# Performance work log

Hardware: AMD Instinct MI355X
Metric: run time of the kernel (lower is better)

Reference implementation:

```python
import jax, jax.numpy as jnp
import numpy as np

B, N, K = 4, 8192, 16
D_POINTS, D_MODEL, INIT_DIM = 64, 64, 3

def _lin(key, din, dout, bias=True):
    k1, k2 = jax.random.split(key)
    s = 1.0 / np.sqrt(din)
    w = jax.random.uniform(k1, (din, dout), minval=-s, maxval=s, dtype=jnp.float32)
    if not bias:
        return w
    b = jax.random.uniform(k2, (dout,), minval=-s, maxval=s, dtype=jnp.float32)
    return w, b

def setup_inputs() -> dict:
    key = jax.random.key(0)
    ks = jax.random.split(key, 12)
    xyz = jax.random.normal(ks[0], (B, N, INIT_DIM), dtype=jnp.float32)
    features = jax.random.normal(ks[1], (B, N, D_POINTS), dtype=jnp.float32)
    knn_idx = jax.random.randint(ks[2], (B, N, K), 0, N)
    fc1_w, fc1_b = _lin(ks[3], D_POINTS, D_MODEL)
    fc2_w, fc2_b = _lin(ks[4], D_MODEL, D_POINTS)
    d1_w, d1_b = _lin(ks[5], INIT_DIM, D_MODEL)
    d2_w, d2_b = _lin(ks[6], D_MODEL, D_MODEL)
    g1_w, g1_b = _lin(ks[7], D_MODEL, D_MODEL)
    g2_w, g2_b = _lin(ks[8], D_MODEL, D_MODEL)
    wq = _lin(ks[9], D_MODEL, D_MODEL, bias=False)
    wk = _lin(ks[10], D_MODEL, D_MODEL, bias=False)
    wv = _lin(ks[11], D_MODEL, D_MODEL, bias=False)
    return dict(xyz=xyz, features=features, knn_idx=knn_idx,
                fc1_w=fc1_w, fc1_b=fc1_b, fc2_w=fc2_w, fc2_b=fc2_b,
                d1_w=d1_w, d1_b=d1_b, d2_w=d2_w, d2_b=d2_b,
                g1_w=g1_w, g1_b=g1_b, g2_w=g2_w, g2_b=g2_b,
                wq=wq, wk=wk, wv=wv)

def _index_points(x, idx):
    # x: (B, N, D), idx: (B, M, K) -> (B, M, K, D)
    return jax.vmap(lambda xb, ib: xb[ib])(x, idx)

def reference(xyz, features, knn_idx,
              fc1_w, fc1_b, fc2_w, fc2_b,
              d1_w, d1_b, d2_w, d2_b,
              g1_w, g1_b, g2_w, g2_b,
              wq, wk, wv):
    idx = knn_idx[:, :, :K]
    knn_xyz = _index_points(xyz, idx)                      # (B,N,K,3)
    pre = features
    x = features @ fc1_w + fc1_b                           # (B,N,d_model)
    q = x @ wq                                             # (B,N,d_model)
    k = _index_points(x @ wk, idx)                         # (B,N,K,d_model)
    v = _index_points(x @ wv, idx)                         # (B,N,K,d_model)
    rel = xyz[:, :, None, :] - knn_xyz                     # (B,N,K,3)
    pos_enc = jax.nn.relu(rel @ d1_w + d1_b) @ d2_w + d2_b # (B,N,K,d_model)
    h = q[:, :, None, :] - k + pos_enc
    attn = jax.nn.relu(h @ g1_w + g1_b) @ g2_w + g2_b      # (B,N,K,d_model)
    attn = jax.nn.softmax(attn / np.sqrt(D_MODEL), axis=-2)
    res = jnp.einsum('bmnf,bmnf->bmf', attn, v + pos_enc)  # (B,N,d_model)
    res = res @ fc2_w + fc2_b + pre                        # (B,N,d_points)
    return res, attn
```

## Files before the change

kernel.cpp:

```cpp
#include <hip/hip_runtime.h>
#include <hip/hip_bf16.h>

#define B_    4
#define N_    8192
#define TOT   (B_*N_)
#define KNN_  16
#define PPW   8
#define PITCH 80

typedef _Float16 half8  __attribute__((ext_vector_type(8)));
typedef float    floatx4 __attribute__((ext_vector_type(4)));

#define MFMA16(A, Bv, C) __builtin_amdgcn_mfma_f32_16x16x32_f16((A), (Bv), (C), 0, 0, 0)

__device__ __forceinline__ void lds_fence(){
  asm volatile("s_waitcnt lgkmcnt(0)" ::: "memory");
}
__device__ __forceinline__ half8 h8_load_f32(const float* __restrict__ p){
  float4 a = *(const float4*)p;
  float4 b = *(const float4*)(p + 4);
  half8 r;
  r[0] = (_Float16)a.x; r[1] = (_Float16)a.y; r[2] = (_Float16)a.z; r[3] = (_Float16)a.w;
  r[4] = (_Float16)b.x; r[5] = (_Float16)b.y; r[6] = (_Float16)b.z; r[7] = (_Float16)b.w;
  return r;
}
__device__ __forceinline__ void store8f(float* __restrict__ p, half8 v){
  float4 a = {(float)v[0], (float)v[1], (float)v[2], (float)v[3]};
  float4 b = {(float)v[4], (float)v[5], (float)v[6], (float)v[7]};
  *(float4*)p = a;
  *(float4*)(p + 4) = b;
}

__device__ void fill_w64(half8* dst, const float* __restrict__ W, int tid){
  for (int i = tid; i < 512; i += 256){
    int lane = i & 63, nt = (i >> 6) & 3, kt = i >> 8;
    int n  = nt*16 + (lane & 15);
    int kb = kt*32 + ((lane >> 4) & 3)*8;
    half8 v;
    #pragma unroll
    for (int j = 0; j < 8; j++) v[j] = (_Float16)W[(kb + j)*64 + n];
    dst[i] = v;
  }
}

__global__ __launch_bounds__(256, 3) void k1_qkv(
    const float* __restrict__ feat, const float* __restrict__ fc1w, const float* __restrict__ fc1b,
    const float* __restrict__ wqw, const float* __restrict__ wkw, const float* __restrict__ wvw,
    _Float16* __restrict__ qws, _Float16* __restrict__ kws, _Float16* __restrict__ vws)
{
  __shared__ half8 Sfc1[512], Sq[512], Sk[512], Sv[512];
  __shared__ alignas(16) _Float16 xt[4][16*PITCH];
  const int tid = threadIdx.x;
  fill_w64(Sfc1, fc1w, tid);
  fill_w64(Sq, wqw, tid);
  fill_w64(Sk, wkw, tid);
  fill_w64(Sv, wvw, tid);
  __syncthreads();

  const int wave = tid >> 6, lane = tid & 63, quad = lane >> 4, m16 = lane & 15;
  _Float16* tx = &xt[wave][0];
  const int rowbase = blockIdx.x*64 + wave*16;
  float fb[4];
  #pragma unroll
  for (int nt = 0; nt < 4; nt++) fb[nt] = fc1b[nt*16 + m16];

  const int arow = rowbase + m16;
  half8 Fa0 = h8_load_f32(&feat[arow*64 + quad*8]);
  half8 Fa1 = h8_load_f32(&feat[arow*64 + 32 + quad*8]);
  const floatx4 z4 = {0.f, 0.f, 0.f, 0.f};

  #pragma unroll
  for (int nt = 0; nt < 4; nt++){
    floatx4 acc = MFMA16(Fa0, Sfc1[nt*64 + lane], z4);
    acc = MFMA16(Fa1, Sfc1[(4 + nt)*64 + lane], acc);
    const int col = nt*16 + m16;
    #pragma unroll
    for (int r = 0; r < 4; r++)
      tx[(quad*4 + r)*PITCH + col] = (_Float16)(acc[r] + fb[nt]);
  }
  lds_fence();
  const half8 Ax0 = *(const half8*)&tx[m16*PITCH + quad*8];
  const half8 Ax1 = *(const half8*)&tx[m16*PITCH + 32 + quad*8];

#define EMIT_QKV(S, OUT)                                                      \
  { _Pragma("unroll")                                                         \
    for (int nt = 0; nt < 4; nt++){                                           \
      floatx4 acc = MFMA16(Ax0, S[nt*64 + lane], z4);                         \
      acc = MFMA16(Ax1, S[(4 + nt)*64 + lane], acc);                          \
      _Pragma("unroll")                                                       \
      for (int r = 0; r < 4; r++)                                             \
        OUT[(rowbase + quad*4 + r)*64 + nt*16 + m16] = (_Float16)acc[r];      \
    } }
  EMIT_QKV(Sq, qws)
  EMIT_QKV(Sk, kws)
  EMIT_QKV(Sv, vws)
#undef EMIT_QKV
}

__global__ __launch_bounds__(256, 2) void k2_point(
    const float* __restrict__ xyz, const int* __restrict__ knn,
    const float* __restrict__ d1w, const float* __restrict__ d1b,
    const float* __restrict__ d2w, const float* __restrict__ d2b,
    const float* __restrict__ g1w, const float* __restrict__ g1b,
    const float* __restrict__ g2w, const float* __restrict__ g2b,
    const _Float16* __restrict__ qws, const _Float16* __restrict__ kws,
    const _Float16* __restrict__ vws,
    _Float16* __restrict__ r0, float* __restrict__ attn_out)
{
  __shared__ half8 Sd2[512], Sg1[512], Sg2[512];
  __shared__ float4 Td1[64];
  __shared__ alignas(16) _Float16 tiles[4][2][16*PITCH];
  const int tid = threadIdx.x;
  fill_w64(Sd2, d2w, tid);
  fill_w64(Sg1, g1w, tid);
  fill_w64(Sg2, g2w, tid);
  if (tid < 64)
    Td1[tid] = make_float4(d1w[tid], d1w[64 + tid], d1w[128 + tid], d1b[tid]);
  __syncthreads();

  const int wave = tid >> 6, lane = tid & 63, quad = lane >> 4, m16 = lane & 15;
  _Float16* tT0 = &tiles[wave][0][0];
  _Float16* tT1 = &tiles[wave][1][0];

  half8 Fd2[2][4], Fg1[2][4], Fg2[2][4];
  #pragma unroll
  for (int nt = 0; nt < 4; nt++){
    #pragma unroll
    for (int kt = 0; kt < 2; kt++){
      Fd2[kt][nt] = Sd2[(kt*4 + nt)*64 + lane];
      Fg1[kt][nt] = Sg1[(kt*4 + nt)*64 + lane];
      Fg2[kt][nt] = Sg2[(kt*4 + nt)*64 + lane];
    }
  }
  float bd2[4], bg1[4], bg2[4];
  #pragma unroll
  for (int nt = 0; nt < 4; nt++){
    const int c = nt*16 + m16;
    bd2[nt] = d2b[c]; bg1[nt] = g1b[c]; bg2[nt] = g2b[c];
  }
  const floatx4 z4 = {0.f, 0.f, 0.f, 0.f};
  const int wsw = quad << 3;
  const int swz = (quad ^ (m16 >> 2)) << 3;

  const int swb  = (blockIdx.x & 7)*128 + (blockIdx.x >> 3);
  const int gpt0 = swb*(4*PPW) + wave*PPW;
  const int b    = gpt0 >> 13;

  int growA = b*N_ + knn[gpt0*KNN_ + m16];
  int growB = b*N_ + knn[(gpt0+1)*KNN_ + m16];
  float xqA0 = xyz[gpt0*3+0],     xqA1 = xyz[gpt0*3+1],     xqA2 = xyz[gpt0*3+2];
  float xqB0 = xyz[(gpt0+1)*3+0], xqB1 = xyz[(gpt0+1)*3+1], xqB2 = xyz[(gpt0+1)*3+2];
  float xnA0 = xyz[growA*3+0], xnA1 = xyz[growA*3+1], xnA2 = xyz[growA*3+2];
  float xnB0 = xyz[growB*3+0], xnB1 = xyz[growB*3+1], xnB2 = xyz[growB*3+2];

  for (int pp = 0; pp < PPW; pp += 2){
    const int gptA = gpt0 + pp, gptB = gptA + 1;
    const int gA = growA, gB = growB;

    const half8 KaA0 = *(const half8*)&kws[gA*64 + quad*8];
    const half8 KaA1 = *(const half8*)&kws[gA*64 + 32 + quad*8];
    const half8 QaA0 = *(const half8*)&qws[gptA*64 + quad*8];
    const half8 QaA1 = *(const half8*)&qws[gptA*64 + 32 + quad*8];
    const half8 VaA0 = *(const half8*)&vws[gA*64 + quad*8];
    const half8 VaA1 = *(const half8*)&vws[gA*64 + 32 + quad*8];
    const half8 KaB0 = *(const half8*)&kws[gB*64 + quad*8];
    const half8 KaB1 = *(const half8*)&kws[gB*64 + 32 + quad*8];
    const half8 QaB0 = *(const half8*)&qws[gptB*64 + quad*8];
    const half8 QaB1 = *(const half8*)&qws[gptB*64 + 32 + quad*8];
    const half8 VaB0 = *(const half8*)&vws[gB*64 + quad*8];
    const half8 VaB1 = *(const half8*)&vws[gB*64 + 32 + quad*8];

    int growA_n = 0, growB_n = 0;
    if (pp < PPW-2){
      growA_n = b*N_ + knn[(gptA+2)*KNN_ + m16];
      growB_n = b*N_ + knn[(gptB+2)*KNN_ + m16];
    }

    const float dxA = xqA0 - xnA0, dyA = xqA1 - xnA1, dzA = xqA2 - xnA2;
    const float dxB = xqB0 - xnB0, dyB = xqB1 - xnB1, dzB = xqB2 - xnB2;

    half8 AtA0, AtA1, AtB0, AtB1;
    #pragma unroll
    for (int j = 0; j < 8; j++){
      const float4 w  = Td1[quad*8 + j];
      const float4 w2 = Td1[32 + quad*8 + j];
      float tA  = fmaf(dxA, w.x,  fmaf(dyA, w.y,  fmaf(dzA, w.z,  w.w)));
      float tA2 = fmaf(dxA, w2.x, fmaf(dyA, w2.y, fmaf(dzA, w2.z, w2.w)));
      float tB  = fmaf(dxB, w.x,  fmaf(dyB, w.y,  fmaf(dzB, w.z,  w.w)));
      float tB2 = fmaf(dxB, w2.x, fmaf(dyB, w2.y, fmaf(dzB, w2.z, w2.w)));
      AtA0[j] = (_Float16)(tA  > 0.f ? tA  : 0.f);
      AtA1[j] = (_Float16)(tA2 > 0.f ? tA2 : 0.f);
      AtB0[j] = (_Float16)(tB  > 0.f ? tB  : 0.f);
      AtB1[j] = (_Float16)(tB2 > 0.f ? tB2 : 0.f);
    }

    #pragma unroll
    for (int nt = 0; nt < 4; nt++){
      floatx4 accA = MFMA16(AtA0, Fd2[0][nt], z4);
      accA = MFMA16(AtA1, Fd2[1][nt], accA);
      floatx4 accB = MFMA16(AtB0, Fd2[0][nt], z4);
      accB = MFMA16(AtB1, Fd2[1][nt], accB);
      const int colS = (nt*16 + m16) ^ wsw;
      #pragma unroll
      for (int r = 0; r < 4; r++){
        tT0[(quad*4 + r)*PITCH + colS] = (_Float16)(accA[r] + bd2[nt]);
        tT1[(quad*4 + r)*PITCH + colS] = (_Float16)(accB[r] + bd2[nt]);
      }
    }
    lds_fence();
    const half8 PaA0 = *(const half8*)&tT0[m16*PITCH + swz];
    const half8 PaA1 = *(const half8*)&tT0[m16*PITCH + 32 + swz];
    const half8 PaB0 = *(const half8*)&tT1[m16*PITCH + swz];
    const half8 PaB1 = *(const half8*)&tT1[m16*PITCH + 32 + swz];
    const half8 HA0 = QaA0 - KaA0 + PaA0;
    const half8 HA1 = QaA1 - KaA1 + PaA1;
    const half8 HB0 = QaB0 - KaB0 + PaB0;
    const half8 HB1 = QaB1 - KaB1 + PaB1;

    #pragma unroll
    for (int nt = 0; nt < 4; nt++){
      floatx4 accA = MFMA16(HA0, Fg1[0][nt], z4);
      accA = MFMA16(HA1, Fg1[1][nt], accA);
      floatx4 accB = MFMA16(HB0, Fg1[0][nt], z4);
      accB = MFMA16(HB1, Fg1[1][nt], accB);
      const int colS = (nt*16 + m16) ^ wsw;
      #pragma unroll
      for (int r = 0; r < 4; r++){
        float tA = accA[r] + bg1[nt];
        float tB = accB[r] + bg1[nt];
        tT0[(quad*4 + r)*PITCH + colS] = (_Float16)(tA > 0.f ? tA : 0.f);
        tT1[(quad*4 + r)*PITCH + colS] = (_Float16)(tB > 0.f ? tB : 0.f);
      }
    }
    lds_fence();
    const half8 UA0 = *(const half8*)&tT0[m16*PITCH + swz];
    const half8 UA1 = *(const half8*)&tT0[m16*PITCH + 32 + swz];
    const half8 UB0 = *(const half8*)&tT1[m16*PITCH + swz];
    const half8 UB1 = *(const half8*)&tT1[m16*PITCH + 32 + swz];

    float A2A[4][4], A2B[4][4];
    #pragma unroll
    for (int nt = 0; nt < 4; nt++){
      floatx4 accA = MFMA16(UA0, Fg2[0][nt], z4);
      accA = MFMA16(UA1, Fg2[1][nt], accA);
      floatx4 accB = MFMA16(UB0, Fg2[0][nt], z4);
      accB = MFMA16(UB1, Fg2[1][nt], accB);
      #pragma unroll
      for (int r = 0; r < 4; r++){ A2A[nt][r] = accA[r] + bg2[nt]; A2B[nt][r] = accB[r] + bg2[nt]; }
    }
    #pragma unroll
    for (int nt = 0; nt < 4; nt++){
      float mxA = fmaxf(fmaxf(A2A[nt][0], A2A[nt][1]), fmaxf(A2A[nt][2], A2A[nt][3]));
      float mxB = fmaxf(fmaxf(A2B[nt][0], A2B[nt][1]), fmaxf(A2B[nt][2], A2B[nt][3]));
      mxA = fmaxf(mxA, __shfl_xor(mxA, 16));
      mxB = fmaxf(mxB, __shfl_xor(mxB, 16));
      mxA = fmaxf(mxA, __shfl_xor(mxA, 32));
      mxB = fmaxf(mxB, __shfl_xor(mxB, 32));
      float sA = 0.f, sB = 0.f;
      #pragma unroll
      for (int r = 0; r < 4; r++){
        float eA = exp2f((A2A[nt][r] - mxA)*0.18033688011112042f);
        float eB = exp2f((A2B[nt][r] - mxB)*0.18033688011112042f);
        A2A[nt][r] = eA; sA += eA;
        A2B[nt][r] = eB; sB += eB;
      }
      sA += __shfl_xor(sA, 16);
      sB += __shfl_xor(sB, 16);
      sA += __shfl_xor(sA, 32);
      sB += __shfl_xor(sB, 32);
      const float invA = __builtin_amdgcn_rcpf(sA);
      const float invB = __builtin_amdgcn_rcpf(sB);
      const int colS = (nt*16 + m16) ^ wsw;
      #pragma unroll
      for (int r = 0; r < 4; r++){
        tT0[(quad*4 + r)*PITCH + colS] = (_Float16)(A2A[nt][r]*invA);
        tT1[(quad*4 + r)*PITCH + colS] = (_Float16)(A2B[nt][r]*invB);
      }
    }
    lds_fence();
    const half8 AaA0 = *(const half8*)&tT0[m16*PITCH + swz];
    const half8 AaA1 = *(const half8*)&tT0[m16*PITCH + 32 + swz];
    const half8 AaB0 = *(const half8*)&tT1[m16*PITCH + swz];
    const half8 AaB1 = *(const half8*)&tT1[m16*PITCH + 32 + swz];

    float* apA = attn_out + ((size_t)gptA*KNN_ + m16)*64;
    store8f(apA + quad*8, AaA0);
    store8f(apA + 32 + quad*8, AaA1);
    float* apB = attn_out + ((size_t)gptB*KNN_ + m16)*64;
    store8f(apB + quad*8, AaB0);
    store8f(apB + 32 + quad*8, AaB1);

    float w0[8], w1[8], y0[8], y1[8];
    #pragma unroll
    for (int j = 0; j < 8; j++){
      w0[j] = (float)AaA0[j] * ((float)VaA0[j] + (float)PaA0[j]);
      w1[j] = (float)AaA1[j] * ((float)VaA1[j] + (float)PaA1[j]);
      y0[j] = (float)AaB0[j] * ((float)VaB0[j] + (float)PaB0[j]);
      y1[j] = (float)AaB1[j] * ((float)VaB1[j] + (float)PaB1[j]);
    }
    #pragma unroll
    for (int mask = 1; mask < 16; mask <<= 1){
      #pragma unroll
      for (int j = 0; j < 8; j++){
        w0[j] += __shfl_xor(w0[j], mask);
        w1[j] += __shfl_xor(w1[j], mask);
        y0[j] += __shfl_xor(y0[j], mask);
        y1[j] += __shfl_xor(y1[j], mask);
      }
    }
    if (m16 == 0){
      half8 oA0, oA1, oB0, oB1;
      #pragma unroll
      for (int j = 0; j < 8; j++){
        oA0[j] = (_Float16)w0[j]; oA1[j] = (_Float16)w1[j];
        oB0[j] = (_Float16)y0[j]; oB1[j] = (_Float16)y1[j];
      }
      *(half8*)&r0[gptA*64 + quad*8] = oA0;
      *(half8*)&r0[gptA*64 + 32 + quad*8] = oA1;
      *(half8*)&r0[gptB*64 + quad*8] = oB0;
      *(half8*)&r0[gptB*64 + 32 + quad*8] = oB1;
    }

    if (pp < PPW-2){
      growA = growA_n; growB = growB_n;
      xqA0 = xyz[(gptA+2)*3+0]; xqA1 = xyz[(gptA+2)*3+1]; xqA2 = xyz[(gptA+2)*3+2];
      xqB0 = xyz[(gptB+2)*3+0]; xqB1 = xyz[(gptB+2)*3+1]; xqB2 = xyz[(gptB+2)*3+2];
      xnA0 = xyz[growA_n*3+0]; xnA1 = xyz[growA_n*3+1]; xnA2 = xyz[growA_n*3+2];
      xnB0 = xyz[growB_n*3+0]; xnB1 = xyz[growB_n*3+1]; xnB2 = xyz[growB_n*3+2];
    }
  }
}

__global__ __launch_bounds__(256, 2) void k3_fc2(
    const _Float16* __restrict__ r0, const float* __restrict__ fc2w,
    const float* __restrict__ fc2b, const float* __restrict__ feat,
    float* __restrict__ out_res)
{
  __shared__ half8 S[512];
  const int tid = threadIdx.x;
  fill_w64(S, fc2w, tid);
  __syncthreads();

  const int wave = tid >> 6, lane = tid & 63, quad = lane >> 4, m16 = lane & 15;
  const int rowbase = blockIdx.x*64 + wave*16;
  float fb[4];
  #pragma unroll
  for (int nt = 0; nt < 4; nt++) fb[nt] = fc2b[nt*16 + m16];

  const half8 A0 = *(const half8*)&r0[(rowbase + m16)*64 + quad*8];
  const half8 A1 = *(const half8*)&r0[(rowbase + m16)*64 + 32 + quad*8];
  const floatx4 z4 = {0.f, 0.f, 0.f, 0.f};

  #pragma unroll
  for (int nt = 0; nt < 4; nt++){
    floatx4 acc = MFMA16(A0, S[nt*64 + lane], z4);
    acc = MFMA16(A1, S[(4 + nt)*64 + lane], acc);
    #pragma unroll
    for (int r = 0; r < 4; r++){
      const int rowg = rowbase + quad*4 + r;
      const int col  = nt*16 + m16;
      out_res[rowg*64 + col] = acc[r] + fb[nt] + feat[rowg*64 + col];
    }
  }
}

extern "C" void kernel_launch(void* const* d_in, const int* in_sizes, int n_in,
                              void* d_out, int out_size, void* d_ws, size_t ws_size,
                              hipStream_t stream)
{
  (void)in_sizes; (void)n_in; (void)out_size; (void)ws_size;
  const float* xyz  = (const float*)d_in[0];
  const float* feat = (const float*)d_in[1];
  const int*   knn  = (const int*)d_in[2];
  const float* fc1w = (const float*)d_in[3];
  const float* fc1b = (const float*)d_in[4];
  const float* fc2w = (const float*)d_in[5];
  const float* fc2b = (const float*)d_in[6];
  const float* d1w  = (const float*)d_in[7];
  const float* d1b  = (const float*)d_in[8];
  const float* d2w  = (const float*)d_in[9];
  const float* d2b  = (const float*)d_in[10];
  const float* g1w  = (const float*)d_in[11];
  const float* g1b  = (const float*)d_in[12];
  const float* g2w  = (const float*)d_in[13];
  const float* g2b  = (const float*)d_in[14];
  const float* wq   = (const float*)d_in[15];
  const float* wk   = (const float*)d_in[16];
  const float* wv   = (const float*)d_in[17];

  _Float16* ws  = (_Float16*)d_ws;
  _Float16* qws = ws;
  _Float16* kws = ws + (size_t)TOT*64;
  _Float16* vws = ws + (size_t)2*TOT*64;
  _Float16* r0  = ws + (size_t)3*TOT*64;

  float* out      = (float*)d_out;
  float* out_res  = out;
  float* out_attn = out + (size_t)TOT*64;

  k1_qkv<<<TOT/64, 256, 0, stream>>>(feat, fc1w, fc1b, wq, wk, wv, qws, kws, vws);
  k2_point<<<TOT/(4*PPW), 256, 0, stream>>>(xyz, knn, d1w, d1b, d2w, d2b,
                                            g1w, g1b, g2w, g2b,
                                            qws, kws, vws, r0, out_attn);
  k3_fc2<<<TOT/64, 256, 0, stream>>>(r0, fc2w, fc2b, feat, out_res);
}
```

Measured before the change: 255.4 us.

## Compute attention-weighted sum in MFMA layout and defer attn stores one iteration

The weighted sum over neighbours is now computed straight from the MFMA accumulator layout. V is gathered per column with scalar loads, and the reduction uses a two-step cross-quad shuffle instead of a 4-step xor over 16 lanes on 32 values. The attention tile goes to a separate LDS buffer and is written to global memory during the next iteration, so that memory traffic overlaps compute and one LDS fence/read per iteration is dropped. In exchange, the scalar fp16 V gathers are less coalesced, LDS use grows, and more registers are held live.

```diff
diff --git a/kernel.cpp b/kernel.cpp
--- a/kernel.cpp
+++ b/kernel.cpp
@@ -110,6 +110,7 @@
   __shared__ half8 Sd2[512], Sg1[512], Sg2[512];
   __shared__ float4 Td1[64];
   __shared__ alignas(16) _Float16 tiles[4][2][16*PITCH];
+  __shared__ alignas(16) _Float16 atile[4][2][16*PITCH];
   const int tid = threadIdx.x;
   fill_w64(Sd2, d2w, tid);
   fill_w64(Sg1, g1w, tid);
@@ -121,6 +122,8 @@
   const int wave = tid >> 6, lane = tid & 63, quad = lane >> 4, m16 = lane & 15;
   _Float16* tT0 = &tiles[wave][0][0];
   _Float16* tT1 = &tiles[wave][1][0];
+  _Float16* aT0 = &atile[wave][0][0];
+  _Float16* aT1 = &atile[wave][1][0];
 
   half8 Fd2[2][4], Fg1[2][4], Fg2[2][4];
   #pragma unroll
@@ -153,6 +156,8 @@
   float xnA0 = xyz[growA*3+0], xnA1 = xyz[growA*3+1], xnA2 = xyz[growA*3+2];
   float xnB0 = xyz[growB*3+0], xnB1 = xyz[growB*3+1], xnB2 = xyz[growB*3+2];
 
+  int prevA = -1, prevB = -1;
+
   for (int pp = 0; pp < PPW; pp += 2){
     const int gptA = gpt0 + pp, gptB = gptA + 1;
     const int gA = growA, gB = growB;
@@ -161,14 +166,24 @@
     const half8 KaA1 = *(const half8*)&kws[gA*64 + 32 + quad*8];
     const half8 QaA0 = *(const half8*)&qws[gptA*64 + quad*8];
     const half8 QaA1 = *(const half8*)&qws[gptA*64 + 32 + quad*8];
-    const half8 VaA0 = *(const half8*)&vws[gA*64 + quad*8];
-    const half8 VaA1 = *(const half8*)&vws[gA*64 + 32 + quad*8];
     const half8 KaB0 = *(const half8*)&kws[gB*64 + quad*8];
     const half8 KaB1 = *(const half8*)&kws[gB*64 + 32 + quad*8];
     const half8 QaB0 = *(const half8*)&qws[gptB*64 + quad*8];
     const half8 QaB1 = *(const half8*)&qws[gptB*64 + 32 + quad*8];
-    const half8 VaB0 = *(const half8*)&vws[gB*64 + quad*8];
-    const half8 VaB1 = *(const half8*)&vws[gB*64 + 32 + quad*8];
+
+    const int gA0 = __shfl(gA, quad*4 + 0), gA1 = __shfl(gA, quad*4 + 1);
+    const int gA2 = __shfl(gA, quad*4 + 2), gA3 = __shfl(gA, quad*4 + 3);
+    const int gB0 = __shfl(gB, quad*4 + 0), gB1 = __shfl(gB, quad*4 + 1);
+    const int gB2 = __shfl(gB, quad*4 + 2), gB3 = __shfl(gB, quad*4 + 3);
+    _Float16 VcA[4][4], VcB[4][4];
+    #pragma unroll
+    for (int nt = 0; nt < 4; nt++){
+      const int c = nt*16 + m16;
+      VcA[nt][0] = vws[gA0*64 + c]; VcA[nt][1] = vws[gA1*64 + c];
+      VcA[nt][2] = vws[gA2*64 + c]; VcA[nt][3] = vws[gA3*64 + c];
+      VcB[nt][0] = vws[gB0*64 + c]; VcB[nt][1] = vws[gB1*64 + c];
+      VcB[nt][2] = vws[gB2*64 + c]; VcB[nt][3] = vws[gB3*64 + c];
+    }
 
     int growA_n = 0, growB_n = 0;
     if (pp < PPW-2){
@@ -194,6 +209,7 @@
       AtB1[j] = (_Float16)(tB2 > 0.f ? tB2 : 0.f);
     }
 
+    float PcA[4][4], PcB[4][4];
     #pragma unroll
     for (int nt = 0; nt < 4; nt++){
       floatx4 accA = MFMA16(AtA0, Fd2[0][nt], z4);
@@ -203,11 +219,27 @@
       const int colS = (nt*16 + m16) ^ wsw;
       #pragma unroll
       for (int r = 0; r < 4; r++){
-        tT0[(quad*4 + r)*PITCH + colS] = (_Float16)(accA[r] + bd2[nt]);
-        tT1[(quad*4 + r)*PITCH + colS] = (_Float16)(accB[r] + bd2[nt]);
+        PcA[nt][r] = accA[r] + bd2[nt];
+        PcB[nt][r] = accB[r] + bd2[nt];
+        tT0[(quad*4 + r)*PITCH + colS] = (_Float16)PcA[nt][r];
+        tT1[(quad*4 + r)*PITCH + colS] = (_Float16)PcB[nt][r];
       }
     }
     lds_fence();
+
+    if (prevA >= 0){
+      const half8 pA0 = *(const half8*)&aT0[m16*PITCH + swz];
+      const half8 pA1 = *(const half8*)&aT0[m16*PITCH + 32 + swz];
+      const half8 pB0 = *(const half8*)&aT1[m16*PITCH + swz];
+      const half8 pB1 = *(const half8*)&aT1[m16*PITCH + 32 + swz];
+      float* apA = attn_out + ((size_t)prevA*KNN_ + m16)*64;
+      store8f(apA + quad*8, pA0);
+      store8f(apA + 32 + quad*8, pA1);
+      float* apB = attn_out + ((size_t)prevB*KNN_ + m16)*64;
+      store8f(apB + quad*8, pB0);
+      store8f(apB + 32 + quad*8, pB1);
+    }
+
     const half8 PaA0 = *(const half8*)&tT0[m16*PITCH + swz];
     const half8 PaA1 = *(const half8*)&tT0[m16*PITCH + 32 + swz];
     const half8 PaB0 = *(const half8*)&tT1[m16*PITCH + swz];
@@ -270,56 +302,37 @@
       sB += __shfl_xor(sB, 32);
       const float invA = __builtin_amdgcn_rcpf(sA);
       const float invB = __builtin_amdgcn_rcpf(sB);
+      #pragma unroll
+      for (int r = 0; r < 4; r++){ A2A[nt][r] *= invA; A2B[nt][r] *= invB; }
       const int colS = (nt*16 + m16) ^ wsw;
       #pragma unroll
       for (int r = 0; r < 4; r++){
-        tT0[(quad*4 + r)*PITCH + colS] = (_Float16)(A2A[nt][r]*invA);
-        tT1[(quad*4 + r)*PITCH + colS] = (_Float16)(A2B[nt][r]*invB);
+        aT0[(quad*4 + r)*PITCH + colS] = (_Float16)A2A[nt][r];
+        aT1[(quad*4 + r)*PITCH + colS] = (_Float16)A2B[nt][r];
       }
     }
-    lds_fence();
-    const half8 AaA0 = *(const half8*)&tT0[m16*PITCH + swz];
-    const half8 AaA1 = *(const half8*)&tT0[m16*PITCH + 32 + swz];
-    const half8 AaB0 = *(const half8*)&tT1[m16*PITCH + swz];
-    const half8 AaB1 = *(const half8*)&tT1[m16*PITCH + 32 + swz];
-
-    float* apA = attn_out + ((size_t)gptA*KNN_ + m16)*64;
-    store8f(apA + quad*8, AaA0);
-    store8f(apA + 32 + quad*8, AaA1);
-    float* apB = attn_out + ((size_t)gptB*KNN_ + m16)*64;
-    store8f(apB + quad*8, AaB0);
-    store8f(apB + 32 + quad*8, AaB1);
-
-    float w0[8], w1[8], y0[8], y1[8];
-    #pragma unroll
-    for (int j = 0; j < 8; j++){
-      w0[j] = (float)AaA0[j] * ((float)VaA0[j] + (float)PaA0[j]);
-      w1[j] = (float)AaA1[j] * ((float)VaA1[j] + (float)PaA1[j]);
-      y0[j] = (float)AaB0[j] * ((float)VaB0[j] + (float)PaB0[j]);
-      y1[j] = (float)AaB1[j] * ((float)VaB1[j] + (float)PaB1[j]);
-    }
-    #pragma unroll
-    for (int mask = 1; mask < 16; mask <<= 1){
-      #pragma unroll
-      for (int j = 0; j < 8; j++){
-        w0[j] += __shfl_xor(w0[j], mask);
-        w1[j] += __shfl_xor(w1[j], mask);
-        y0[j] += __shfl_xor(y0[j], mask);
-        y1[j] += __shfl_xor(y1[j], mask);
+
+    #pragma unroll
+    for (int nt = 0; nt < 4; nt++){
+      float sA = A2A[nt][0]*((float)VcA[nt][0] + PcA[nt][0])
+               + A2A[nt][1]*((float)VcA[nt][1] + PcA[nt][1])
+               + A2A[nt][2]*((float)VcA[nt][2] + PcA[nt][2])
+               + A2A[nt][3]*((float)VcA[nt][3] + PcA[nt][3]);
+      float sB = A2B[nt][0]*((float)VcB[nt][0] + PcB[nt][0])
+               + A2B[nt][1]*((float)VcB[nt][1] + PcB[nt][1])
+               + A2B[nt][2]*((float)VcB[nt][2] + PcB[nt][2])
+               + A2B[nt][3]*((float)VcB[nt][3] + PcB[nt][3]);
+      sA += __shfl_xor(sA, 16);
+      sB += __shfl_xor(sB, 16);
+      sA += __shfl_xor(sA, 32);
+      sB += __shfl_xor(sB, 32);
+      if (quad == 0){
+        r0[gptA*64 + nt*16 + m16] = (_Float16)sA;
+        r0[gptB*64 + nt*16 + m16] = (_Float16)sB;
       }
     }
-    if (m16 == 0){
-      half8 oA0, oA1, oB0, oB1;
-      #pragma unroll
-      for (int j = 0; j < 8; j++){
-        oA0[j] = (_Float16)w0[j]; oA1[j] = (_Float16)w1[j];
-        oB0[j] = (_Float16)y0[j]; oB1[j] = (_Float16)y1[j];
-      }
-      *(half8*)&r0[gptA*64 + quad*8] = oA0;
-      *(half8*)&r0[gptA*64 + 32 + quad*8] = oA1;
-      *(half8*)&r0[gptB*64 + quad*8] = oB0;
-      *(half8*)&r0[gptB*64 + 32 + quad*8] = oB1;
-    }
+
+    prevA = gptA; prevB = gptB;
 
     if (pp < PPW-2){
       growA = growA_n; growB = growB_n;
@@ -328,6 +341,20 @@
       xnA0 = xyz[growA_n*3+0]; xnA1 = xyz[growA_n*3+1]; xnA2 = xyz[growA_n*3+2];
       xnB0 = xyz[growB_n*3+0]; xnB1 = xyz[growB_n*3+1]; xnB2 = xyz[growB_n*3+2];
     }
+  }
+
+  lds_fence();
+  {
+    const half8 pA0 = *(const half8*)&aT0[m16*PITCH + swz];
+    const half8 pA1 = *(const half8*)&aT0[m16*PITCH + 32 + swz];
+    const half8 pB0 = *(const half8*)&aT1[m16*PITCH + swz];
+    const half8 pB1 = *(const half8*)&aT1[m16*PITCH + 32 + swz];
+    float* apA = attn_out + ((size_t)prevA*KNN_ + m16)*64;
+    store8f(apA + quad*8, pA0);
+    store8f(apA + 32 + quad*8, pA1);
+    float* apB = attn_out + ((size_t)prevB*KNN_ + m16)*64;
+    store8f(apB + quad*8, pB0);
+    store8f(apB + 32 + quad*8, pB1);
   }
 }
 
```

Result: no change. 251.0 us (-1.7%).
